# Performance work log

Hardware: AMD Instinct MI355X
Metric: run time of the kernel (lower is better)

The kernel has to match this reference:

```python
import jax, jax.numpy as jnp
import numpy as np

NUM_EXPERTS = 8
TOP_K = 2
D_MODEL = 1024
D_FF = 4096
B, S = 2, 2048


def setup_inputs() -> dict:
    key = jax.random.key(0)
    k1, k2, k3, k4 = jax.random.split(key, 4)
    scale_in = 1.0 / np.sqrt(D_MODEL)
    scale_ff = 1.0 / np.sqrt(D_FF)
    return {
        "hidden_states": jax.random.normal(k1, (B, S, D_MODEL), dtype=jnp.float32),
        "gate_w": jax.random.normal(k2, (D_MODEL, NUM_EXPERTS), dtype=jnp.float32) * scale_in,
        "w1": jax.random.normal(k3, (NUM_EXPERTS, D_MODEL, D_FF), dtype=jnp.float32) * scale_in,
        "w2": jax.random.normal(k4, (NUM_EXPERTS, D_FF, D_MODEL), dtype=jnp.float32) * scale_ff,
    }


def reference(hidden_states, gate_w, w1, w2):
    b, s, d = hidden_states.shape
    x = hidden_states.reshape(-1, d)                      # [T, d]
    gate_logits = x @ gate_w                              # [T, E]
    top_vals, top_idx = jax.lax.top_k(gate_logits, TOP_K)  # [T, K]
    # softmax over selected expert logits in fp32, cast back
    top_w = jax.nn.softmax(top_vals.astype(jnp.float32), axis=1).astype(x.dtype)
    # per-token per-expert combine weight: sum_k w[t,k] * (sel[t,k]==e)
    combine = jnp.einsum("tke,tk->te", jax.nn.one_hot(top_idx, NUM_EXPERTS, dtype=x.dtype), top_w)  # [T, E]
    # naive dense MoE: every expert over all tokens (matches torch loop)
    h = jax.nn.relu(jnp.einsum("td,edf->etf", x, w1))     # [E, T, d_ff]
    expert_out = jnp.einsum("etf,efd->etd", h, w2)        # [E, T, d]
    final = jnp.einsum("etd,te->td", expert_out, combine)  # [T, d]
    return final.reshape(b, s, d)
```

## Files before the change

### kernel.cpp

```cpp
#include <hip/hip_runtime.h>
#include <hip/hip_bf16.h>
#include <stdint.h>


#define T_TOK 4096
#define DM 1024
#define DF 4096
#define NE 8
#define BM 128
#define BN 128
#define BK 64
#define MAX_TILES 72
#define PAIR_CAP 9216

typedef __bf16 bf16x8 __attribute__((ext_vector_type(8)));
typedef float f32x4 __attribute__((ext_vector_type(4)));
typedef unsigned short ushort_t;

__device__ __forceinline__ ushort_t f2bf(float f) {
  uint32_t u = __float_as_uint(f);
  u += 0x7FFFu + ((u >> 16) & 1u);
  return (ushort_t)(u >> 16);
}

#define WT_OFF  0ull
#define XB_OFF  67108864ull
#define H_OFF   75497472ull
#define RT_OFF  201326592ull
#define RO_COUNTS   0
#define RO_OFFSETS  32
#define RO_CURSORS  64
#define RO_NTILES   96
#define RO_TILE_E   128
#define RO_TILE_S   448
#define RO_TILE_R   768
#define RO_PTOK     1088
#define RO_PW       37952
#define RO_TOPI     74816
#define RO_TOPW     107584
#define RT_BYTES    140352ull
#define WS_NEEDED   (RT_OFF + RT_BYTES)

__device__ __forceinline__ int xcd_work(int b, int live) {
  int k = b & 7, j = b >> 3;
  int q = live >> 3, r = live & 7;
  int cnt = q + (k < r ? 1 : 0);
  if (j >= cnt) return -1;
  int start = k * q + (k < r ? k : r);
  return start + j;
}

__global__ void gate_kernel(const float* __restrict__ x, const float* __restrict__ gw,
                            int* __restrict__ counts, int* __restrict__ topi,
                            float* __restrict__ topw, ushort_t* __restrict__ xb) {
  int wave = threadIdx.x >> 6;
  int lane = threadIdx.x & 63;
  int t = blockIdx.x * 4 + wave;
  const float* xr = x + (size_t)t * DM;
  ushort_t* xbr = xb + (size_t)t * DM;
  float acc[NE];
#pragma unroll
  for (int e = 0; e < NE; ++e) acc[e] = 0.f;
#pragma unroll
  for (int it = 0; it < DM / 256; ++it) {
    int d0 = (it * 64 + lane) * 4;
    float4 v = *(const float4*)&xr[d0];
    ushort4 o = { f2bf(v.x), f2bf(v.y), f2bf(v.z), f2bf(v.w) };
    *(ushort4*)&xbr[d0] = o;
    const float* g0 = gw + (size_t)d0 * NE;
#pragma unroll
    for (int e = 0; e < NE; ++e)
      acc[e] += v.x * g0[e] + v.y * g0[NE + e] + v.z * g0[2 * NE + e] + v.w * g0[3 * NE + e];
  }
#pragma unroll
  for (int off = 32; off > 0; off >>= 1) {
#pragma unroll
    for (int e = 0; e < NE; ++e) acc[e] += __shfl_xor(acc[e], off, 64);
  }
  if (lane == 0) {
    int i0 = 0; float v0 = acc[0];
#pragma unroll
    for (int e = 1; e < NE; ++e) if (acc[e] > v0) { v0 = acc[e]; i0 = e; }
    int i1 = -1; float v1 = -1e30f;
#pragma unroll
    for (int e = 0; e < NE; ++e) if (e != i0 && acc[e] > v1) { v1 = acc[e]; i1 = e; }
    float e1 = expf(v1 - v0);
    float w0 = 1.f / (1.f + e1);
    float w1 = e1 / (1.f + e1);
    topi[t * 2] = i0; topi[t * 2 + 1] = i1;
    topw[t * 2] = w0; topw[t * 2 + 1] = w1;
    atomicAdd(&counts[i0], 1);
    atomicAdd(&counts[i1], 1);
  }
}

__global__ void scan_kernel(const int* __restrict__ counts, int* __restrict__ offsets,
                            int* __restrict__ cursors, int* __restrict__ n_tiles,
                            int* __restrict__ tile_e, int* __restrict__ tile_s,
                            int* __restrict__ tile_r) {
  if (threadIdx.x == 0) {
    int off = 0, nt = 0;
    for (int e = 0; e < NE; ++e) {
      offsets[e] = off;
      cursors[e] = 0;
      int c = counts[e];
      for (int m0 = 0; m0 < c; m0 += BM) {
        tile_e[nt] = e;
        tile_s[nt] = off + m0;
        tile_r[nt] = (c - m0 < BM) ? (c - m0) : BM;
        ++nt;
      }
      off += ((c + BM - 1) / BM) * BM;
    }
    *n_tiles = nt;
  }
}

__global__ void scatter_kernel(const int* __restrict__ topi, const float* __restrict__ topw,
                               const int* __restrict__ offsets, int* __restrict__ cursors,
                               int* __restrict__ ptok, float* __restrict__ pw) {
  int t = blockIdx.x * 256 + threadIdx.x;
  if (t >= T_TOK) return;
#pragma unroll
  for (int k = 0; k < 2; ++k) {
    int e = topi[t * 2 + k];
    int pos = atomicAdd(&cursors[e], 1);
    int p = offsets[e] + pos;
    ptok[p] = t;
    pw[p] = topw[t * 2 + k];
  }
}

__global__ void transpose_convert(const float* __restrict__ src, ushort_t* __restrict__ dst,
                                  int R, int C) {
  __shared__ ushort_t tile[64][136];
  int e = blockIdx.z;
  src += (size_t)e * R * C;
  dst += (size_t)e * R * C;
  int c0 = blockIdx.x * 64, r0 = blockIdx.y * 128;
  int tr = threadIdx.x >> 4;
  int tc = (threadIdx.x & 15) << 2;
#pragma unroll
  for (int i = 0; i < 8; ++i) {
    int r = i * 16 + tr;
    float4 v = *(const float4*)&src[(size_t)(r0 + r) * C + c0 + tc];
    tile[tc + 0][r] = f2bf(v.x);
    tile[tc + 1][r] = f2bf(v.y);
    tile[tc + 2][r] = f2bf(v.z);
    tile[tc + 3][r] = f2bf(v.w);
  }
  __syncthreads();
  int cr = threadIdx.x >> 5;
  int rg = (threadIdx.x & 31) << 2;
#pragma unroll
  for (int j = 0; j < 8; ++j) {
    int c = j * 8 + cr;
    ushort4 o = { tile[c][rg], tile[c][rg + 1], tile[c][rg + 2], tile[c][rg + 3] };
    *(ushort4*)&dst[(size_t)(c0 + c) * R + r0 + rg] = o;
  }
}


#define GLD(srcp, dstp)                                                        \
  __builtin_amdgcn_global_load_lds(                                            \
      (const __attribute__((address_space(1))) void*)(srcp),                   \
      (__attribute__((address_space(3))) void*)(dstp), 16, 0, 0)

__device__ __forceinline__ void gemm_core(
    ushort_t* As, ushort_t* Bs,
    const ushort_t* const (&a_sp)[4], const ushort_t* const (&b_sp)[4],
    int NT, int wid, int lane, f32x4 (&acc)[4][4]) {
  int fr = lane & 15, ch = lane >> 4, sw = lane & 7;
  int k0s = (ch ^ sw) * 8;
  int k1s = ((ch + 4) ^ sw) * 8;
  int m_off = (wid >> 1) * 64, n_off = (wid & 1) * 64;
  int abase = (m_off + fr) * 64;
  int bbase = (n_off + fr) * 64;

  for (int t = 0; t < NT; ++t) {
    int k0 = t * BK;
#pragma unroll
    for (int j = 0; j < 4; ++j) {
      GLD(a_sp[j] + k0, As + (wid * 4 + j) * 512);
      GLD(b_sp[j] + k0, Bs + (wid * 4 + j) * 512);
    }
    asm volatile("s_waitcnt vmcnt(0)" ::: "memory");
    __syncthreads();

#pragma unroll
    for (int kx = 0; kx < 2; ++kx) {
      int ks = kx ? k1s : k0s;
      bf16x8 af[4], bf[4];
#pragma unroll
      for (int mi = 0; mi < 4; ++mi) af[mi] = *(const bf16x8*)&As[abase + mi * 1024 + ks];
#pragma unroll
      for (int ni = 0; ni < 4; ++ni) bf[ni] = *(const bf16x8*)&Bs[bbase + ni * 1024 + ks];
#pragma unroll
      for (int mi = 0; mi < 4; ++mi)
#pragma unroll
        for (int ni = 0; ni < 4; ++ni)
          acc[mi][ni] = __builtin_amdgcn_mfma_f32_16x16x32_bf16(af[mi], bf[ni], acc[mi][ni], 0, 0, 0);
    }
    __syncthreads();
  }
}

__global__ __launch_bounds__(256, 4) void gemm1_kernel(
    const ushort_t* __restrict__ xb, const ushort_t* __restrict__ w1t,
    ushort_t* __restrict__ h,
    const int* __restrict__ n_tiles, const int* __restrict__ tile_e,
    const int* __restrict__ tile_s, const int* __restrict__ tile_r,
    const int* __restrict__ ptok) {
  int work = xcd_work(blockIdx.x, *n_tiles * (DF / BN));
  if (work < 0) return;
  int tile = work >> 5;
  int n0 = (work & 31) * BN;
  int e = tile_e[tile], p0 = tile_s[tile], rows = tile_r[tile];

  __shared__ ushort_t As[BM * BK];
  __shared__ ushort_t Bs[BN * BK];
  int tid = threadIdx.x, wid = tid >> 6, lane = tid & 63;
  int lr = lane >> 3;
  int swc = (lane & 7) ^ (lr & 7);

  const ushort_t* a_sp[4];
  const ushort_t* b_sp[4];
#pragma unroll
  for (int j = 0; j < 4; ++j) {
    int r = wid * 32 + j * 8 + lr;
    int tok = (r < rows) ? ptok[p0 + r] : 0;
    a_sp[j] = xb + (size_t)tok * DM + swc * 8;
    b_sp[j] = w1t + ((size_t)e * DF + n0 + r) * DM + swc * 8;
  }

  f32x4 acc[4][4] = {};
  gemm_core(As, Bs, a_sp, b_sp, DM / BK, wid, lane, acc);

  int m_off = (wid >> 1) * 64, n_off = (wid & 1) * 64;
  int col = lane & 15, rq = (lane >> 4) * 4;
#pragma unroll
  for (int mi = 0; mi < 4; ++mi)
#pragma unroll
    for (int r = 0; r < 4; ++r) {
      int m = m_off + mi * 16 + rq + r;
      bool valid = m < rows;
      size_t rowoff = (size_t)(p0 + m) * DF + n0 + n_off;
#pragma unroll
      for (int ni = 0; ni < 4; ++ni) {
        float v = acc[mi][ni][r];
        v = valid ? (v > 0.f ? v : 0.f) : 0.f;
        h[rowoff + ni * 16 + col] = f2bf(v);
      }
    }
}

__global__ __launch_bounds__(256, 4) void gemm2_kernel(
    const ushort_t* __restrict__ h, const ushort_t* __restrict__ w2t,
    float* __restrict__ out,
    const int* __restrict__ n_tiles, const int* __restrict__ tile_e,
    const int* __restrict__ tile_s, const int* __restrict__ tile_r,
    const int* __restrict__ ptok, const float* __restrict__ pw) {
  int work = xcd_work(blockIdx.x, *n_tiles * (DM / BN));
  if (work < 0) return;
  int tile = work >> 3;
  int n0 = (work & 7) * BN;
  int e = tile_e[tile], p0 = tile_s[tile], rows = tile_r[tile];

  __shared__ ushort_t As[BM * BK];
  __shared__ ushort_t Bs[BN * BK];
  int tid = threadIdx.x, wid = tid >> 6, lane = tid & 63;
  int lr = lane >> 3;
  int swc = (lane & 7) ^ (lr & 7);

  const ushort_t* a_sp[4];
  const ushort_t* b_sp[4];
#pragma unroll
  for (int j = 0; j < 4; ++j) {
    int r = wid * 32 + j * 8 + lr;
    a_sp[j] = h + (size_t)(p0 + r) * DF + swc * 8;
    b_sp[j] = w2t + ((size_t)e * DM + n0 + r) * DF + swc * 8;
  }

  f32x4 acc[4][4] = {};
  gemm_core(As, Bs, a_sp, b_sp, DF / BK, wid, lane, acc);

  int m_off = (wid >> 1) * 64, n_off = (wid & 1) * 64;
  int col = lane & 15, rq = (lane >> 4) * 4;
#pragma unroll
  for (int mi = 0; mi < 4; ++mi)
#pragma unroll
    for (int r = 0; r < 4; ++r) {
      int m = m_off + mi * 16 + rq + r;
      if (m < rows) {
        int p = p0 + m;
        int tok = ptok[p];
        float w = pw[p];
        size_t o = (size_t)tok * DM + n0 + n_off;
#pragma unroll
        for (int ni = 0; ni < 4; ++ni)
          atomicAdd(&out[o + ni * 16 + col], w * acc[mi][ni][r]);
      }
    }
}

extern "C" void kernel_launch(void* const* d_in, const int* in_sizes, int n_in,
                              void* d_out, int out_size, void* d_ws, size_t ws_size,
                              hipStream_t stream) {
  const float* x  = (const float*)d_in[0];
  const float* gw = (const float*)d_in[1];
  const float* w1 = (const float*)d_in[2];
  const float* w2 = (const float*)d_in[3];
  float* out = (float*)d_out;
  char* ws = (char*)d_ws;
  if (ws_size < WS_NEEDED) return;

  ushort_t* wt  = (ushort_t*)(ws + WT_OFF);
  ushort_t* xb  = (ushort_t*)(ws + XB_OFF);
  ushort_t* h   = (ushort_t*)(ws + H_OFF);
  char* rt = ws + RT_OFF;
  int*   counts  = (int*)(rt + RO_COUNTS);
  int*   offsets = (int*)(rt + RO_OFFSETS);
  int*   cursors = (int*)(rt + RO_CURSORS);
  int*   n_tiles = (int*)(rt + RO_NTILES);
  int*   tile_e  = (int*)(rt + RO_TILE_E);
  int*   tile_s  = (int*)(rt + RO_TILE_S);
  int*   tile_r  = (int*)(rt + RO_TILE_R);
  int*   ptok    = (int*)(rt + RO_PTOK);
  float* pw      = (float*)(rt + RO_PW);
  int*   topi    = (int*)(rt + RO_TOPI);
  float* topw    = (float*)(rt + RO_TOPW);

  hipMemsetAsync(rt, 0, 128, stream);
  hipMemsetAsync(out, 0, (size_t)T_TOK * DM * sizeof(float), stream);

  hipLaunchKernelGGL(gate_kernel, dim3(T_TOK / 4), dim3(256), 0, stream,
                     x, gw, counts, topi, topw, xb);
  hipLaunchKernelGGL(scan_kernel, dim3(1), dim3(64), 0, stream,
                     counts, offsets, cursors, n_tiles, tile_e, tile_s, tile_r);
  hipLaunchKernelGGL(scatter_kernel, dim3(T_TOK / 256), dim3(256), 0, stream,
                     topi, topw, offsets, cursors, ptok, pw);
  hipLaunchKernelGGL(transpose_convert, dim3(DF / 64, DM / 128, NE), dim3(256), 0, stream,
                     w1, wt, DM, DF);
  hipLaunchKernelGGL(gemm1_kernel, dim3(MAX_TILES * (DF / BN)), dim3(256), 0, stream,
                     xb, wt, h, n_tiles, tile_e, tile_s, tile_r, ptok);
  hipLaunchKernelGGL(transpose_convert, dim3(DM / 64, DF / 128, NE), dim3(256), 0, stream,
                     w2, wt, DF, DM);
  hipLaunchKernelGGL(gemm2_kernel, dim3(MAX_TILES * (DM / BN)), dim3(256), 0, stream,
                     h, wt, out, n_tiles, tile_e, tile_s, tile_r, ptok, pw);
}
```

Measured before the change: 422.1 us.

## Merge routing kernels, fuse weight transposes, and group GEMM tiles for L2 reuse

Scan and scatter are merged into one single-block route kernel that uses shared-memory cursors, and the two weight transpose/convert launches become one kernel writing into separate buffers. This cuts launch count and moves the W2 conversion ahead of gemm1, at the cost of a larger workspace. Both GEMMs now remap work indices so that neighbouring blocks share a group of row tiles and column tiles, which is meant to improve L2 reuse of weights and activations. The route kernel runs serially on a single block over 4096 tokens, which may take longer than the previous multi-block scatter.

```diff
diff --git a/kernel.cpp b/kernel.cpp
--- a/kernel.cpp
+++ b/kernel.cpp
@@ -23,13 +23,12 @@
   return (ushort_t)(u >> 16);
 }
 
-#define WT_OFF  0ull
-#define XB_OFF  67108864ull
-#define H_OFF   75497472ull
-#define RT_OFF  201326592ull
+#define W1T_OFF 0ull
+#define W2T_OFF 67108864ull
+#define XB_OFF  134217728ull
+#define H_OFF   142606336ull
+#define RT_OFF  218103808ull
 #define RO_COUNTS   0
-#define RO_OFFSETS  32
-#define RO_CURSORS  64
 #define RO_NTILES   96
 #define RO_TILE_E   128
 #define RO_TILE_S   448
@@ -94,15 +93,18 @@
   }
 }
 
-__global__ void scan_kernel(const int* __restrict__ counts, int* __restrict__ offsets,
-                            int* __restrict__ cursors, int* __restrict__ n_tiles,
-                            int* __restrict__ tile_e, int* __restrict__ tile_s,
-                            int* __restrict__ tile_r) {
+__global__ void route_kernel(const int* __restrict__ counts,
+                             const int* __restrict__ topi, const float* __restrict__ topw,
+                             int* __restrict__ n_tiles, int* __restrict__ tile_e,
+                             int* __restrict__ tile_s, int* __restrict__ tile_r,
+                             int* __restrict__ ptok, float* __restrict__ pw) {
+  __shared__ int loff[NE];
+  __shared__ int lcur[NE];
   if (threadIdx.x == 0) {
     int off = 0, nt = 0;
     for (int e = 0; e < NE; ++e) {
-      offsets[e] = off;
-      cursors[e] = 0;
+      loff[e] = off;
+      lcur[e] = 0;
       int c = counts[e];
       for (int m0 = 0; m0 < c; m0 += BM) {
         tile_e[nt] = e;
@@ -114,30 +116,37 @@
     }
     *n_tiles = nt;
   }
-}
-
-__global__ void scatter_kernel(const int* __restrict__ topi, const float* __restrict__ topw,
-                               const int* __restrict__ offsets, int* __restrict__ cursors,
-                               int* __restrict__ ptok, float* __restrict__ pw) {
-  int t = blockIdx.x * 256 + threadIdx.x;
-  if (t >= T_TOK) return;
-#pragma unroll
-  for (int k = 0; k < 2; ++k) {
-    int e = topi[t * 2 + k];
-    int pos = atomicAdd(&cursors[e], 1);
-    int p = offsets[e] + pos;
-    ptok[p] = t;
-    pw[p] = topw[t * 2 + k];
-  }
-}
-
-__global__ void transpose_convert(const float* __restrict__ src, ushort_t* __restrict__ dst,
-                                  int R, int C) {
+  __syncthreads();
+  for (int t = threadIdx.x; t < T_TOK; t += 256) {
+#pragma unroll
+    for (int k = 0; k < 2; ++k) {
+      int e = topi[t * 2 + k];
+      int pos = atomicAdd(&lcur[e], 1);
+      int p = loff[e] + pos;
+      ptok[p] = t;
+      pw[p] = topw[t * 2 + k];
+    }
+  }
+}
+
+__global__ void transpose_all(const float* __restrict__ w1, const float* __restrict__ w2,
+                              ushort_t* __restrict__ w1t, ushort_t* __restrict__ w2t) {
   __shared__ ushort_t tile[64][136];
-  int e = blockIdx.z;
+  int b = blockIdx.x;
+  const float* src; ushort_t* dst; int R, C, bx, by, e;
+  if (b < 4096) {
+    e = b >> 9; int t2 = b & 511;
+    bx = t2 & 63; by = t2 >> 6;
+    src = w1; dst = w1t; R = DM; C = DF;
+  } else {
+    b -= 4096;
+    e = b >> 9; int t2 = b & 511;
+    bx = t2 & 15; by = t2 >> 4;
+    src = w2; dst = w2t; R = DF; C = DM;
+  }
   src += (size_t)e * R * C;
   dst += (size_t)e * R * C;
-  int c0 = blockIdx.x * 64, r0 = blockIdx.y * 128;
+  int c0 = bx * 64, r0 = by * 128;
   int tr = threadIdx.x >> 4;
   int tc = (threadIdx.x & 15) << 2;
 #pragma unroll
@@ -211,10 +220,15 @@
     const int* __restrict__ n_tiles, const int* __restrict__ tile_e,
     const int* __restrict__ tile_s, const int* __restrict__ tile_r,
     const int* __restrict__ ptok) {
-  int work = xcd_work(blockIdx.x, *n_tiles * (DF / BN));
-  if (work < 0) return;
-  int tile = work >> 5;
-  int n0 = (work & 31) * BN;
+  int nt = *n_tiles;
+  int ntp = (nt + 3) & ~3;
+  int w = xcd_work(blockIdx.x, ntp * 32);
+  if (w < 0) return;
+  int g = w >> 5, r = w & 31;
+  int tg = g >> 2, ng = g & 3;
+  int tile = tg * 4 + (r & 3);
+  if (tile >= nt) return;
+  int n0 = (ng * 8 + (r >> 2)) * BN;
   int e = tile_e[tile], p0 = tile_s[tile], rows = tile_r[tile];
 
   __shared__ ushort_t As[BM * BK];
@@ -227,10 +241,10 @@
   const ushort_t* b_sp[4];
 #pragma unroll
   for (int j = 0; j < 4; ++j) {
-    int r = wid * 32 + j * 8 + lr;
-    int tok = (r < rows) ? ptok[p0 + r] : 0;
+    int rr = wid * 32 + j * 8 + lr;
+    int tok = (rr < rows) ? ptok[p0 + rr] : 0;
     a_sp[j] = xb + (size_t)tok * DM + swc * 8;
-    b_sp[j] = w1t + ((size_t)e * DF + n0 + r) * DM + swc * 8;
+    b_sp[j] = w1t + ((size_t)e * DF + n0 + rr) * DM + swc * 8;
   }
 
   f32x4 acc[4][4] = {};
@@ -241,13 +255,13 @@
 #pragma unroll
   for (int mi = 0; mi < 4; ++mi)
 #pragma unroll
-    for (int r = 0; r < 4; ++r) {
-      int m = m_off + mi * 16 + rq + r;
+    for (int rr = 0; rr < 4; ++rr) {
+      int m = m_off + mi * 16 + rq + rr;
       bool valid = m < rows;
       size_t rowoff = (size_t)(p0 + m) * DF + n0 + n_off;
 #pragma unroll
       for (int ni = 0; ni < 4; ++ni) {
-        float v = acc[mi][ni][r];
+        float v = acc[mi][ni][rr];
         v = valid ? (v > 0.f ? v : 0.f) : 0.f;
         h[rowoff + ni * 16 + col] = f2bf(v);
       }
@@ -260,10 +274,15 @@
     const int* __restrict__ n_tiles, const int* __restrict__ tile_e,
     const int* __restrict__ tile_s, const int* __restrict__ tile_r,
     const int* __restrict__ ptok, const float* __restrict__ pw) {
-  int work = xcd_work(blockIdx.x, *n_tiles * (DM / BN));
-  if (work < 0) return;
-  int tile = work >> 3;
-  int n0 = (work & 7) * BN;
+  int nt = *n_tiles;
+  int ntp = (nt + 1) & ~1;
+  int w = xcd_work(blockIdx.x, ntp * 8);
+  if (w < 0) return;
+  int g = w >> 2, r = w & 3;
+  int tg = g >> 2, ng = g & 3;
+  int tile = tg * 2 + (r & 1);
+  if (tile >= nt) return;
+  int n0 = (ng * 2 + (r >> 1)) * BN;
   int e = tile_e[tile], p0 = tile_s[tile], rows = tile_r[tile];
 
   __shared__ ushort_t As[BM * BK];
@@ -276,9 +295,9 @@
   const ushort_t* b_sp[4];
 #pragma unroll
   for (int j = 0; j < 4; ++j) {
-    int r = wid * 32 + j * 8 + lr;
-    a_sp[j] = h + (size_t)(p0 + r) * DF + swc * 8;
-    b_sp[j] = w2t + ((size_t)e * DM + n0 + r) * DF + swc * 8;
+    int rr = wid * 32 + j * 8 + lr;
+    a_sp[j] = h + (size_t)(p0 + rr) * DF + swc * 8;
+    b_sp[j] = w2t + ((size_t)e * DM + n0 + rr) * DF + swc * 8;
   }
 
   f32x4 acc[4][4] = {};
@@ -289,16 +308,16 @@
 #pragma unroll
   for (int mi = 0; mi < 4; ++mi)
 #pragma unroll
-    for (int r = 0; r < 4; ++r) {
-      int m = m_off + mi * 16 + rq + r;
+    for (int rr = 0; rr < 4; ++rr) {
+      int m = m_off + mi * 16 + rq + rr;
       if (m < rows) {
         int p = p0 + m;
         int tok = ptok[p];
-        float w = pw[p];
+        float wgt = pw[p];
         size_t o = (size_t)tok * DM + n0 + n_off;
 #pragma unroll
         for (int ni = 0; ni < 4; ++ni)
-          atomicAdd(&out[o + ni * 16 + col], w * acc[mi][ni][r]);
+          atomicAdd(&out[o + ni * 16 + col], wgt * acc[mi][ni][rr]);
       }
     }
 }
@@ -314,13 +333,12 @@
   char* ws = (char*)d_ws;
   if (ws_size < WS_NEEDED) return;
 
-  ushort_t* wt  = (ushort_t*)(ws + WT_OFF);
+  ushort_t* w1t = (ushort_t*)(ws + W1T_OFF);
+  ushort_t* w2t = (ushort_t*)(ws + W2T_OFF);
   ushort_t* xb  = (ushort_t*)(ws + XB_OFF);
   ushort_t* h   = (ushort_t*)(ws + H_OFF);
   char* rt = ws + RT_OFF;
   int*   counts  = (int*)(rt + RO_COUNTS);
-  int*   offsets = (int*)(rt + RO_OFFSETS);
-  int*   cursors = (int*)(rt + RO_CURSORS);
   int*   n_tiles = (int*)(rt + RO_NTILES);
   int*   tile_e  = (int*)(rt + RO_TILE_E);
   int*   tile_s  = (int*)(rt + RO_TILE_S);
@@ -335,16 +353,12 @@
 
   hipLaunchKernelGGL(gate_kernel, dim3(T_TOK / 4), dim3(256), 0, stream,
                      x, gw, counts, topi, topw, xb);
-  hipLaunchKernelGGL(scan_kernel, dim3(1), dim3(64), 0, stream,
-                     counts, offsets, cursors, n_tiles, tile_e, tile_s, tile_r);
-  hipLaunchKernelGGL(scatter_kernel, dim3(T_TOK / 256), dim3(256), 0, stream,
-                     topi, topw, offsets, cursors, ptok, pw);
-  hipLaunchKernelGGL(transpose_convert, dim3(DF / 64, DM / 128, NE), dim3(256), 0, stream,
-                     w1, wt, DM, DF);
-  hipLaunchKernelGGL(gemm1_kernel, dim3(MAX_TILES * (DF / BN)), dim3(256), 0, stream,
-                     xb, wt, h, n_tiles, tile_e, tile_s, tile_r, ptok);
-  hipLaunchKernelGGL(transpose_convert, dim3(DM / 64, DF / 128, NE), dim3(256), 0, stream,
-                     w2, wt, DF, DM);
-  hipLaunchKernelGGL(gemm2_kernel, dim3(MAX_TILES * (DM / BN)), dim3(256), 0, stream,
-                     h, wt, out, n_tiles, tile_e, tile_s, tile_r, ptok, pw);
-}
+  hipLaunchKernelGGL(route_kernel, dim3(1), dim3(256), 0, stream,
+                     counts, topi, topw, n_tiles, tile_e, tile_s, tile_r, ptok, pw);
+  hipLaunchKernelGGL(transpose_all, dim3(8192), dim3(256), 0, stream,
+                     w1, w2, w1t, w2t);
+  hipLaunchKernelGGL(gemm1_kernel, dim3(MAX_TILES * 32), dim3(256), 0, stream,
+                     xb, w1t, h, n_tiles, tile_e, tile_s, tile_r, ptok);
+  hipLaunchKernelGGL(gemm2_kernel, dim3(MAX_TILES * 8), dim3(256), 0, stream,
+                     h, w2t, out, n_tiles, tile_e, tile_s, tile_r, ptok, pw);
+}
```

New measurement: 384.1 us. -9.0%, faster.
